# Performance work log

Measured on AMD Instinct MI355X. Metric: run time of the kernel, lower is better.

Reference implementation:

```python
import jax, jax.numpy as jnp
import numpy as np

B, T, D, H = 4, 2048, 1024, 16
HD = D // H
K = 4            # templates per token
VOCAB = 32000


def setup_inputs() -> dict:
    key = jax.random.key(0)
    ks = jax.random.split(key, 6)
    x = jax.random.normal(ks[0], (B, T, D), dtype=jnp.float32)
    sequences = jax.random.randint(ks[1], (B, T, K), 0, VOCAB, dtype=jnp.int64)
    # xavier-uniform-ish scaled weights (torch Linear stores [out, in])
    Wqkv = jax.random.normal(ks[2], (3 * D, D), dtype=jnp.float32) * (1.0 / np.sqrt(D))
    Wout = jax.random.normal(ks[3], (D, D), dtype=jnp.float32) * (1.0 / np.sqrt(D))
    bout = jnp.zeros((D,), dtype=jnp.float32)
    emb = jax.random.normal(ks[4], (VOCAB, D), dtype=jnp.float32) * 0.02
    bias_scale = jnp.asarray(0.1, dtype=jnp.float32)
    return {"x": x, "sequences": sequences, "Wqkv": Wqkv, "Wout": Wout,
            "bout": bout, "emb": emb, "bias_scale": bias_scale}


def reference(x, sequences, Wqkv, Wout, bout, emb, bias_scale):
    b, t, d = x.shape
    h, hd = H, d // H
    # qkv projection (no bias): [B,T,3,H,hd]
    qkv = (x @ Wqkv.T).reshape(b, t, 3, h, hd)
    q = jnp.moveaxis(qkv[:, :, 0], 2, 1)  # [B,H,T,hd]
    k = jnp.moveaxis(qkv[:, :, 1], 2, 1)
    v = jnp.moveaxis(qkv[:, :, 2], 2, 1)
    scale = hd ** -0.5
    scores = jnp.einsum('bhqd,bhkd->bhqk', q, k) * scale  # [B,H,T,T]
    causal = jnp.tril(jnp.ones((t, t), dtype=bool))
    scores = jnp.where(causal[None, None], scores, -jnp.inf)
    w = jax.nn.softmax(scores, axis=-1)
    # dropout p=0.0 -> identity (eval-mode faithful)
    out = jnp.einsum('bhqk,bhkd->bhqd', w, v)
    out = jnp.moveaxis(out, 1, 2).reshape(b, t, d)
    # bias injection: sum template embeddings over template axis
    out = out + emb[sequences].sum(axis=-2) * bias_scale
    return out @ Wout.T + bout
```

## Files before the change

kernel.cpp:

```cpp
#include <hip/hip_runtime.h>
#include <stdint.h>


typedef __attribute__((ext_vector_type(8))) short s16x8;
typedef __attribute__((ext_vector_type(4))) short s16x4;
typedef __attribute__((ext_vector_type(4))) float f32x4;

static __device__ __forceinline__ unsigned short f32_bf16(float f) {
  union { float f; unsigned u; } v; v.f = f;
  unsigned r = v.u + 0x7fffu + ((v.u >> 16) & 1u);
  return (unsigned short)(r >> 16);
}
static __device__ __forceinline__ float bf16_f32(unsigned short h) {
  union { float f; unsigned u; } v; v.u = ((unsigned)h) << 16;
  return v.f;
}
static __device__ __forceinline__ float fexp2(float x) {
#if __has_builtin(__builtin_amdgcn_exp2f)
  return __builtin_amdgcn_exp2f(x);
#else
  return exp2f(x);
#endif
}

__global__ __launch_bounds__(256) void cvt_f32_bf16_k(
    const float* __restrict__ in, unsigned short* __restrict__ out, int n8) {
  int i = blockIdx.x * 256 + threadIdx.x;
  if (i >= n8) return;
  const float4* p = (const float4*)(in + (long)i * 8);
  float4 a = p[0], b = p[1];
  s16x8 o;
  o[0] = (short)f32_bf16(a.x); o[1] = (short)f32_bf16(a.y);
  o[2] = (short)f32_bf16(a.z); o[3] = (short)f32_bf16(a.w);
  o[4] = (short)f32_bf16(b.x); o[5] = (short)f32_bf16(b.y);
  o[6] = (short)f32_bf16(b.z); o[7] = (short)f32_bf16(b.w);
  *(s16x8*)(out + (long)i * 8) = o;
}

__device__ __forceinline__ void glds16(const void* g, void* l) {
  __builtin_amdgcn_global_load_lds(
      (const __attribute__((address_space(1))) void*)g,
      (__attribute__((address_space(3))) void*)l, 16, 0, 0);
}

template <int OUTMODE>
__global__ __launch_bounds__(256) void gemm_bt(
    const unsigned short* __restrict__ A,
    const unsigned short* __restrict__ Bm,
    void* __restrict__ C0, void* __restrict__ C1, void* __restrict__ C2,
    const float* __restrict__ bias, int M, int N, int K) {
  __shared__ unsigned short Asl[128 * 32];
  __shared__ unsigned short Bsl[128 * 32];
  const int tid = threadIdx.x;
  const int l = tid & 63;
  const int w = tid >> 6;
  const int wr = w >> 1, wc = w & 1;
  const int bm = blockIdx.y, bn = blockIdx.x;

  f32x4 acc[4][4] = {};

  const unsigned short* Ag = A + (long)(bm * 128 + w * 16 + (l >> 2)) * K + (l & 3) * 8;
  const unsigned short* Bg = Bm + (long)(bn * 128 + w * 16 + (l >> 2)) * K + (l & 3) * 8;
  unsigned short* Al0 = &Asl[w * 512];
  unsigned short* Bl0 = &Bsl[w * 512];
  const int ro = (l & 15) * 32 + (l >> 4) * 8;

  for (int k0 = 0; k0 < K; k0 += 32) {
    __syncthreads();
    glds16(Ag + k0, Al0);
    glds16(Ag + 64 * K + k0, Al0 + 2048);
    glds16(Bg + k0, Bl0);
    glds16(Bg + 64 * K + k0, Bl0 + 2048);
    __syncthreads();
    s16x8 af[4], bfr[4];
#pragma unroll
    for (int i = 0; i < 4; ++i)
      af[i] = *(const s16x8*)&Asl[(wr * 64 + i * 16) * 32 + ro];
#pragma unroll
    for (int j = 0; j < 4; ++j)
      bfr[j] = *(const s16x8*)&Bsl[(wc * 64 + j * 16) * 32 + ro];
#pragma unroll
    for (int i = 0; i < 4; ++i)
#pragma unroll
      for (int j = 0; j < 4; ++j)
        acc[i][j] = __builtin_amdgcn_mfma_f32_16x16x32_bf16(af[i], bfr[j], acc[i][j], 0, 0, 0);
  }

  const int crow = bm * 128 + wr * 64 + (l >> 4) * 4;
  if (OUTMODE == 2) {
    unsigned short* C = (unsigned short*)(bn < 8 ? C0 : (bn < 16 ? C1 : C2));
    const float qsc = (bn < 8) ? 0.18033688f : 1.0f;
    const int colb = (bn & 7) * 128 + wc * 64 + (l & 15);
#pragma unroll
    for (int i = 0; i < 4; ++i)
#pragma unroll
      for (int j = 0; j < 4; ++j)
#pragma unroll
        for (int r = 0; r < 4; ++r)
          C[(long)(crow + i * 16 + r) * 1024 + colb + j * 16] = f32_bf16(acc[i][j][r] * qsc);
  } else {
    float* C = (float*)C0;
    const int ccol = bn * 128 + wc * 64 + (l & 15);
#pragma unroll
    for (int i = 0; i < 4; ++i)
#pragma unroll
      for (int j = 0; j < 4; ++j) {
        float bv = bias[ccol + j * 16];
#pragma unroll
        for (int r = 0; r < 4; ++r)
          C[(long)(crow + i * 16 + r) * N + ccol + j * 16] = acc[i][j][r] + bv;
      }
  }
}


__device__ __forceinline__ void attn_tile(
    const unsigned short* __restrict__ Ksl, const unsigned short* __restrict__ Vtl,
    unsigned short* Psl, const s16x8* qf, f32x4* o, float* m, float* lpart,
    int qt0, int kv0, bool diag, int w, int g, int d15) {
  f32x4 s[4] = {};
  __builtin_amdgcn_s_setprio(1);
#pragma unroll
  for (int st = 0; st < 4; ++st)
#pragma unroll
    for (int kc = 0; kc < 2; ++kc) {
      s16x8 kf = *(const s16x8*)&Ksl[(st * 16 + d15) * 72 + kc * 32 + g * 8];
      s[st] = __builtin_amdgcn_mfma_f32_16x16x32_bf16(qf[kc], kf, s[st], 0, 0, 0);
    }
  __builtin_amdgcn_s_setprio(0);
#pragma unroll
  for (int r = 0; r < 4; ++r) {
    const int qabs = qt0 + w * 16 + g * 4 + r;
    float sv0 = s[0][r], sv1 = s[1][r], sv2 = s[2][r], sv3 = s[3][r];
    if (diag) {
      if (kv0 + d15 > qabs) sv0 = -1e30f;
      if (kv0 + 16 + d15 > qabs) sv1 = -1e30f;
      if (kv0 + 32 + d15 > qabs) sv2 = -1e30f;
      if (kv0 + 48 + d15 > qabs) sv3 = -1e30f;
    }
    float mx = fmaxf(fmaxf(sv0, sv1), fmaxf(sv2, sv3));
    mx = fmaxf(mx, __shfl_xor(mx, 1));
    mx = fmaxf(mx, __shfl_xor(mx, 2));
    mx = fmaxf(mx, __shfl_xor(mx, 4));
    mx = fmaxf(mx, __shfl_xor(mx, 8));
    const float mn = fmaxf(m[r], mx);
    const float c = fexp2(m[r] - mn);
    m[r] = mn;
    const float p0 = fexp2(sv0 - mn), p1 = fexp2(sv1 - mn);
    const float p2 = fexp2(sv2 - mn), p3 = fexp2(sv3 - mn);
    unsigned short* pr = &Psl[(w * 16 + g * 4 + r) * 72 + d15];
    pr[0] = f32_bf16(p0); pr[16] = f32_bf16(p1);
    pr[32] = f32_bf16(p2); pr[48] = f32_bf16(p3);
    lpart[r] = lpart[r] * c + ((p0 + p1) + (p2 + p3));
#pragma unroll
    for (int ct = 0; ct < 4; ++ct) o[ct][r] *= c;
  }
  __builtin_amdgcn_s_setprio(1);
#pragma unroll
  for (int kc2 = 0; kc2 < 2; ++kc2) {
    s16x8 pf = *(const s16x8*)&Psl[(w * 16 + d15) * 72 + kc2 * 32 + g * 8];
#pragma unroll
    for (int ct = 0; ct < 4; ++ct) {
      s16x8 vf = *(const s16x8*)&Vtl[(ct * 16 + d15) * 72 + ((kc2 * 32 + g * 8) ^ (ct * 8))];
      o[ct] = __builtin_amdgcn_mfma_f32_16x16x32_bf16(pf, vf, o[ct], 0, 0, 0);
    }
  }
  __builtin_amdgcn_s_setprio(0);
}

__global__ __launch_bounds__(256) void attn_k(
    const unsigned short* __restrict__ Qb, const unsigned short* __restrict__ Kb,
    const unsigned short* __restrict__ Vb, unsigned short* __restrict__ attn,
    const int* __restrict__ seq, const float* __restrict__ emb,
    const float* __restrict__ bsc) {
  __shared__ unsigned short Ksl[64 * 72];
  __shared__ unsigned short Vtl[64 * 72];
  __shared__ unsigned short Psl[64 * 72];
  const int tid = threadIdx.x;
  const int l = tid & 63;
  const int w = tid >> 6;
  const int g = l >> 4;
  const int d15 = l & 15;
  const int bx = blockIdx.x;
  const int bh = blockIdx.y;
  const int b = bh >> 4, h = bh & 15;
  const int tok0 = b * 2048;
  const int qA = bx, qB = 31 - bx;
  const int nA = qA + 1, ntiles = qB + 1;
  const unsigned short* Qp = Qb + (long)tok0 * 1024 + h * 64;
  const unsigned short* Kp = Kb + (long)tok0 * 1024 + h * 64;
  const unsigned short* Vp = Vb + (long)tok0 * 1024 + h * 64;

  s16x8 qfA[2], qfB[2];
  {
    const unsigned short* qa = Qp + (long)(qA * 64 + w * 16 + d15) * 1024 + g * 8;
    qfA[0] = *(const s16x8*)qa;
    qfA[1] = *(const s16x8*)(qa + 32);
    const unsigned short* qbp = Qp + (long)(qB * 64 + w * 16 + d15) * 1024 + g * 8;
    qfB[0] = *(const s16x8*)qbp;
    qfB[1] = *(const s16x8*)(qbp + 32);
  }
  f32x4 oA[4] = {}, oB[4] = {};
  float mA[4], lA[4], mB[4], lB[4];
#pragma unroll
  for (int r = 0; r < 4; ++r) {
    mA[r] = -1e30f; lA[r] = 0.f; mB[r] = -1e30f; lB[r] = 0.f;
  }

  const int rs_ = tid >> 2;
  const int c0 = (tid & 3) * 16;
  const int vswz = rs_ ^ ((c0 >> 4) * 8);
  const unsigned short* Kg = Kp + (long)rs_ * 1024 + c0;
  const unsigned short* Vg = Vp + (long)rs_ * 1024 + c0;
  s16x8 kp0 = *(const s16x8*)Kg, kp1 = *(const s16x8*)(Kg + 8);
  s16x8 vp0 = *(const s16x8*)Vg, vp1 = *(const s16x8*)(Vg + 8);

  for (int it = 0; it < ntiles; ++it) {
    __syncthreads();
    *(s16x8*)&Ksl[rs_ * 72 + c0] = kp0;
    *(s16x8*)&Ksl[rs_ * 72 + c0 + 8] = kp1;
#pragma unroll
    for (int e = 0; e < 8; ++e) {
      Vtl[(c0 + e) * 72 + vswz] = (unsigned short)vp0[e];
      Vtl[(c0 + 8 + e) * 72 + vswz] = (unsigned short)vp1[e];
    }
    if (it + 1 < ntiles) {
      Kg += 65536; Vg += 65536;
      kp0 = *(const s16x8*)Kg; kp1 = *(const s16x8*)(Kg + 8);
      vp0 = *(const s16x8*)Vg; vp1 = *(const s16x8*)(Vg + 8);
    }
    __syncthreads();
    attn_tile(Ksl, Vtl, Psl, qfB, oB, mB, lB, qB * 64, it * 64, it == qB, w, g, d15);
    if (it < nA)
      attn_tile(Ksl, Vtl, Psl, qfA, oA, mA, lA, qA * 64, it * 64, it == qA, w, g, d15);
  }

#pragma unroll
  for (int r = 0; r < 4; ++r) {
    float sB = lB[r], sA = lA[r];
    sB += __shfl_xor(sB, 1); sB += __shfl_xor(sB, 2);
    sB += __shfl_xor(sB, 4); sB += __shfl_xor(sB, 8);
    sA += __shfl_xor(sA, 1); sA += __shfl_xor(sA, 2);
    sA += __shfl_xor(sA, 4); sA += __shfl_xor(sA, 8);
    lB[r] = sB; lA[r] = sA;
  }

  const float sc = bsc[0];
  const int colbase = h * 64 + d15;
  const int tB0 = tok0 + qB * 64 + w * 16 + g * 4;
  const int tA0 = tok0 + qA * 64 + w * 16 + g * 4;
  unsigned short* apB = attn + (long)tB0 * 1024 + colbase;
  unsigned short* apA = attn + (long)tA0 * 1024 + colbase;
#pragma unroll
  for (int r = 0; r < 4; ++r) {
    const float invB = 1.0f / lB[r];
    const float invA = 1.0f / lA[r];
    const int* sqB = seq + (long)(tB0 + r) * 4;
    const int* sqA = seq + (long)(tA0 + r) * 4;
    const float* eB0 = emb + (long)sqB[0] * 1024 + colbase;
    const float* eB1 = emb + (long)sqB[1] * 1024 + colbase;
    const float* eB2 = emb + (long)sqB[2] * 1024 + colbase;
    const float* eB3 = emb + (long)sqB[3] * 1024 + colbase;
    const float* eA0 = emb + (long)sqA[0] * 1024 + colbase;
    const float* eA1 = emb + (long)sqA[1] * 1024 + colbase;
    const float* eA2 = emb + (long)sqA[2] * 1024 + colbase;
    const float* eA3 = emb + (long)sqA[3] * 1024 + colbase;
#pragma unroll
    for (int ct = 0; ct < 4; ++ct) {
      const int cc = ct * 16;
      float embB = (eB0[cc] + eB1[cc]) + (eB2[cc] + eB3[cc]);
      float embA = (eA0[cc] + eA1[cc]) + (eA2[cc] + eA3[cc]);
      apB[(long)r * 1024 + cc] = f32_bf16(oB[ct][r] * invB + sc * embB);
      apA[(long)r * 1024 + cc] = f32_bf16(oA[ct][r] * invA + sc * embA);
    }
  }
}

extern "C" void kernel_launch(void* const* d_in, const int* in_sizes, int n_in,
                              void* d_out, int out_size, void* d_ws, size_t ws_size,
                              hipStream_t stream) {
  const float* x = (const float*)d_in[0];
  const int* seq = (const int*)d_in[1];
  const float* Wqkv = (const float*)d_in[2];
  const float* Wout = (const float*)d_in[3];
  const float* bout = (const float*)d_in[4];
  const float* emb = (const float*)d_in[5];
  const float* bsc = (const float*)d_in[6];

  uint8_t* ws = (uint8_t*)d_ws;
  unsigned short* xbf = (unsigned short*)ws;
  unsigned short* wqkvb = (unsigned short*)(ws + 16777216);
  unsigned short* woutb = (unsigned short*)(ws + 23068672);
  unsigned short* Qb = (unsigned short*)(ws + 25165824);
  unsigned short* Kb = (unsigned short*)d_out;
  unsigned short* Vb = Kb + (long)8192 * 1024;

  cvt_f32_bf16_k<<<4096, 256, 0, stream>>>(x, xbf, 1048576);
  cvt_f32_bf16_k<<<1536, 256, 0, stream>>>(Wqkv, wqkvb, 393216);
  cvt_f32_bf16_k<<<512, 256, 0, stream>>>(Wout, woutb, 131072);

  gemm_bt<2><<<dim3(24, 64), 256, 0, stream>>>(xbf, wqkvb, Qb, Kb, Vb, nullptr,
                                               8192, 3072, 1024);
  attn_k<<<dim3(16, 64), 256, 0, stream>>>(Qb, Kb, Vb, xbf, seq, emb, bsc);
  gemm_bt<1><<<dim3(8, 64), 256, 0, stream>>>(xbf, woutb, d_out, nullptr, nullptr,
                                              bout, 8192, 1024, 1024);
}
```

Measured before the change: 435.3 us.

## Process four query tiles per attention block, reusing K/V register fragments

Each attention workgroup now handles two 128-row query stripes (four 64-row sub-tiles) paired from opposite ends of the causal triangle instead of two 64-row tiles. K and V fragments are read from LDS into registers once per KV tile and reused across all active sub-tiles, so LDS reads and global K/V loads per query row go down. The grid is halved, which gives fewer blocks per CU. The larger per-thread state (accumulators, Q and K/V fragments) raises register pressure and may lower occupancy or cause spills.

```diff
diff --git a/kernel.cpp b/kernel.cpp
--- a/kernel.cpp
+++ b/kernel.cpp
@@ -113,60 +113,6 @@
   }
 }
 
-
-__device__ __forceinline__ void attn_tile(
-    const unsigned short* __restrict__ Ksl, const unsigned short* __restrict__ Vtl,
-    unsigned short* Psl, const s16x8* qf, f32x4* o, float* m, float* lpart,
-    int qt0, int kv0, bool diag, int w, int g, int d15) {
-  f32x4 s[4] = {};
-  __builtin_amdgcn_s_setprio(1);
-#pragma unroll
-  for (int st = 0; st < 4; ++st)
-#pragma unroll
-    for (int kc = 0; kc < 2; ++kc) {
-      s16x8 kf = *(const s16x8*)&Ksl[(st * 16 + d15) * 72 + kc * 32 + g * 8];
-      s[st] = __builtin_amdgcn_mfma_f32_16x16x32_bf16(qf[kc], kf, s[st], 0, 0, 0);
-    }
-  __builtin_amdgcn_s_setprio(0);
-#pragma unroll
-  for (int r = 0; r < 4; ++r) {
-    const int qabs = qt0 + w * 16 + g * 4 + r;
-    float sv0 = s[0][r], sv1 = s[1][r], sv2 = s[2][r], sv3 = s[3][r];
-    if (diag) {
-      if (kv0 + d15 > qabs) sv0 = -1e30f;
-      if (kv0 + 16 + d15 > qabs) sv1 = -1e30f;
-      if (kv0 + 32 + d15 > qabs) sv2 = -1e30f;
-      if (kv0 + 48 + d15 > qabs) sv3 = -1e30f;
-    }
-    float mx = fmaxf(fmaxf(sv0, sv1), fmaxf(sv2, sv3));
-    mx = fmaxf(mx, __shfl_xor(mx, 1));
-    mx = fmaxf(mx, __shfl_xor(mx, 2));
-    mx = fmaxf(mx, __shfl_xor(mx, 4));
-    mx = fmaxf(mx, __shfl_xor(mx, 8));
-    const float mn = fmaxf(m[r], mx);
-    const float c = fexp2(m[r] - mn);
-    m[r] = mn;
-    const float p0 = fexp2(sv0 - mn), p1 = fexp2(sv1 - mn);
-    const float p2 = fexp2(sv2 - mn), p3 = fexp2(sv3 - mn);
-    unsigned short* pr = &Psl[(w * 16 + g * 4 + r) * 72 + d15];
-    pr[0] = f32_bf16(p0); pr[16] = f32_bf16(p1);
-    pr[32] = f32_bf16(p2); pr[48] = f32_bf16(p3);
-    lpart[r] = lpart[r] * c + ((p0 + p1) + (p2 + p3));
-#pragma unroll
-    for (int ct = 0; ct < 4; ++ct) o[ct][r] *= c;
-  }
-  __builtin_amdgcn_s_setprio(1);
-#pragma unroll
-  for (int kc2 = 0; kc2 < 2; ++kc2) {
-    s16x8 pf = *(const s16x8*)&Psl[(w * 16 + d15) * 72 + kc2 * 32 + g * 8];
-#pragma unroll
-    for (int ct = 0; ct < 4; ++ct) {
-      s16x8 vf = *(const s16x8*)&Vtl[(ct * 16 + d15) * 72 + ((kc2 * 32 + g * 8) ^ (ct * 8))];
-      o[ct] = __builtin_amdgcn_mfma_f32_16x16x32_bf16(pf, vf, o[ct], 0, 0, 0);
-    }
-  }
-  __builtin_amdgcn_s_setprio(0);
-}
 
 __global__ __launch_bounds__(256) void attn_k(
     const unsigned short* __restrict__ Qb, const unsigned short* __restrict__ Kb,
@@ -185,27 +131,33 @@
   const int bh = blockIdx.y;
   const int b = bh >> 4, h = bh & 15;
   const int tok0 = b * 2048;
-  const int qA = bx, qB = 31 - bx;
-  const int nA = qA + 1, ntiles = qB + 1;
+  const int qt_[2] = {15 - bx, bx};
+  const int ntiles = 2 * qt_[0] + 2;
   const unsigned short* Qp = Qb + (long)tok0 * 1024 + h * 64;
   const unsigned short* Kp = Kb + (long)tok0 * 1024 + h * 64;
   const unsigned short* Vp = Vb + (long)tok0 * 1024 + h * 64;
 
-  s16x8 qfA[2], qfB[2];
-  {
-    const unsigned short* qa = Qp + (long)(qA * 64 + w * 16 + d15) * 1024 + g * 8;
-    qfA[0] = *(const s16x8*)qa;
-    qfA[1] = *(const s16x8*)(qa + 32);
-    const unsigned short* qbp = Qp + (long)(qB * 64 + w * 16 + d15) * 1024 + g * 8;
-    qfB[0] = *(const s16x8*)qbp;
-    qfB[1] = *(const s16x8*)(qbp + 32);
-  }
-  f32x4 oA[4] = {}, oB[4] = {};
-  float mA[4], lA[4], mB[4], lB[4];
-#pragma unroll
-  for (int r = 0; r < 4; ++r) {
-    mA[r] = -1e30f; lA[r] = 0.f; mB[r] = -1e30f; lB[r] = 0.f;
-  }
+  s16x8 qf[2][2][2];
+#pragma unroll
+  for (int t = 0; t < 2; ++t)
+#pragma unroll
+    for (int fi = 0; fi < 2; ++fi) {
+      const unsigned short* qr =
+          Qp + (long)(qt_[t] * 128 + fi * 64 + w * 16 + d15) * 1024 + g * 8;
+      qf[t][fi][0] = *(const s16x8*)qr;
+      qf[t][fi][1] = *(const s16x8*)(qr + 32);
+    }
+  f32x4 o[2][2][4] = {};
+  float m[2][2][4], lp[2][2][4];
+#pragma unroll
+  for (int t = 0; t < 2; ++t)
+#pragma unroll
+    for (int fi = 0; fi < 2; ++fi)
+#pragma unroll
+      for (int r = 0; r < 4; ++r) {
+        m[t][fi][r] = -1e30f;
+        lp[t][fi][r] = 0.f;
+      }
 
   const int rs_ = tid >> 2;
   const int c0 = (tid & 3) * 16;
@@ -216,6 +168,7 @@
   s16x8 vp0 = *(const s16x8*)Vg, vp1 = *(const s16x8*)(Vg + 8);
 
   for (int it = 0; it < ntiles; ++it) {
+    const int kv0 = it * 64;
     __syncthreads();
     *(s16x8*)&Ksl[rs_ * 72 + c0] = kp0;
     *(s16x8*)&Ksl[rs_ * 72 + c0 + 8] = kp1;
@@ -230,50 +183,105 @@
       vp0 = *(const s16x8*)Vg; vp1 = *(const s16x8*)(Vg + 8);
     }
     __syncthreads();
-    attn_tile(Ksl, Vtl, Psl, qfB, oB, mB, lB, qB * 64, it * 64, it == qB, w, g, d15);
-    if (it < nA)
-      attn_tile(Ksl, Vtl, Psl, qfA, oA, mA, lA, qA * 64, it * 64, it == qA, w, g, d15);
-  }
-
-#pragma unroll
-  for (int r = 0; r < 4; ++r) {
-    float sB = lB[r], sA = lA[r];
-    sB += __shfl_xor(sB, 1); sB += __shfl_xor(sB, 2);
-    sB += __shfl_xor(sB, 4); sB += __shfl_xor(sB, 8);
-    sA += __shfl_xor(sA, 1); sA += __shfl_xor(sA, 2);
-    sA += __shfl_xor(sA, 4); sA += __shfl_xor(sA, 8);
-    lB[r] = sB; lA[r] = sA;
+
+    s16x8 kf[8], vf[8];
+#pragma unroll
+    for (int st = 0; st < 4; ++st)
+#pragma unroll
+      for (int kc = 0; kc < 2; ++kc)
+        kf[st * 2 + kc] = *(const s16x8*)&Ksl[(st * 16 + d15) * 72 + kc * 32 + g * 8];
+#pragma unroll
+    for (int kc2 = 0; kc2 < 2; ++kc2)
+#pragma unroll
+      for (int ct = 0; ct < 4; ++ct)
+        vf[kc2 * 4 + ct] =
+            *(const s16x8*)&Vtl[(ct * 16 + d15) * 72 + ((kc2 * 32 + g * 8) ^ (ct * 8))];
+
+#pragma unroll
+    for (int t = 0; t < 2; ++t) {
+      const int qt = qt_[t];
+#pragma unroll
+      for (int fi = 0; fi < 2; ++fi) {
+        const int lim = 2 * qt + fi;
+        if (it > lim) continue;
+        const bool diag = (it == lim);
+        f32x4 s[4] = {};
+        __builtin_amdgcn_s_setprio(1);
+#pragma unroll
+        for (int st = 0; st < 4; ++st)
+#pragma unroll
+          for (int kc = 0; kc < 2; ++kc)
+            s[st] = __builtin_amdgcn_mfma_f32_16x16x32_bf16(
+                qf[t][fi][kc], kf[st * 2 + kc], s[st], 0, 0, 0);
+        __builtin_amdgcn_s_setprio(0);
+#pragma unroll
+        for (int r = 0; r < 4; ++r) {
+          const int qabs = qt * 128 + fi * 64 + w * 16 + g * 4 + r;
+          float sv0 = s[0][r], sv1 = s[1][r], sv2 = s[2][r], sv3 = s[3][r];
+          if (diag) {
+            if (kv0 + d15 > qabs) sv0 = -1e30f;
+            if (kv0 + 16 + d15 > qabs) sv1 = -1e30f;
+            if (kv0 + 32 + d15 > qabs) sv2 = -1e30f;
+            if (kv0 + 48 + d15 > qabs) sv3 = -1e30f;
+          }
+          float mx = fmaxf(fmaxf(sv0, sv1), fmaxf(sv2, sv3));
+          mx = fmaxf(mx, __shfl_xor(mx, 1));
+          mx = fmaxf(mx, __shfl_xor(mx, 2));
+          mx = fmaxf(mx, __shfl_xor(mx, 4));
+          mx = fmaxf(mx, __shfl_xor(mx, 8));
+          const float mn = fmaxf(m[t][fi][r], mx);
+          const float c = fexp2(m[t][fi][r] - mn);
+          m[t][fi][r] = mn;
+          const float p0 = fexp2(sv0 - mn), p1 = fexp2(sv1 - mn);
+          const float p2 = fexp2(sv2 - mn), p3 = fexp2(sv3 - mn);
+          unsigned short* pr = &Psl[(w * 16 + g * 4 + r) * 72 + d15];
+          pr[0] = f32_bf16(p0); pr[16] = f32_bf16(p1);
+          pr[32] = f32_bf16(p2); pr[48] = f32_bf16(p3);
+          lp[t][fi][r] = lp[t][fi][r] * c + ((p0 + p1) + (p2 + p3));
+#pragma unroll
+          for (int ct = 0; ct < 4; ++ct) o[t][fi][ct][r] *= c;
+        }
+        __builtin_amdgcn_s_setprio(1);
+#pragma unroll
+        for (int kc2 = 0; kc2 < 2; ++kc2) {
+          s16x8 pf = *(const s16x8*)&Psl[(w * 16 + d15) * 72 + kc2 * 32 + g * 8];
+#pragma unroll
+          for (int ct = 0; ct < 4; ++ct)
+            o[t][fi][ct] = __builtin_amdgcn_mfma_f32_16x16x32_bf16(
+                pf, vf[kc2 * 4 + ct], o[t][fi][ct], 0, 0, 0);
+        }
+        __builtin_amdgcn_s_setprio(0);
+      }
+    }
   }
 
   const float sc = bsc[0];
   const int colbase = h * 64 + d15;
-  const int tB0 = tok0 + qB * 64 + w * 16 + g * 4;
-  const int tA0 = tok0 + qA * 64 + w * 16 + g * 4;
-  unsigned short* apB = attn + (long)tB0 * 1024 + colbase;
-  unsigned short* apA = attn + (long)tA0 * 1024 + colbase;
-#pragma unroll
-  for (int r = 0; r < 4; ++r) {
-    const float invB = 1.0f / lB[r];
-    const float invA = 1.0f / lA[r];
-    const int* sqB = seq + (long)(tB0 + r) * 4;
-    const int* sqA = seq + (long)(tA0 + r) * 4;
-    const float* eB0 = emb + (long)sqB[0] * 1024 + colbase;
-    const float* eB1 = emb + (long)sqB[1] * 1024 + colbase;
-    const float* eB2 = emb + (long)sqB[2] * 1024 + colbase;
-    const float* eB3 = emb + (long)sqB[3] * 1024 + colbase;
-    const float* eA0 = emb + (long)sqA[0] * 1024 + colbase;
-    const float* eA1 = emb + (long)sqA[1] * 1024 + colbase;
-    const float* eA2 = emb + (long)sqA[2] * 1024 + colbase;
-    const float* eA3 = emb + (long)sqA[3] * 1024 + colbase;
-#pragma unroll
-    for (int ct = 0; ct < 4; ++ct) {
-      const int cc = ct * 16;
-      float embB = (eB0[cc] + eB1[cc]) + (eB2[cc] + eB3[cc]);
-      float embA = (eA0[cc] + eA1[cc]) + (eA2[cc] + eA3[cc]);
-      apB[(long)r * 1024 + cc] = f32_bf16(oB[ct][r] * invB + sc * embB);
-      apA[(long)r * 1024 + cc] = f32_bf16(oA[ct][r] * invA + sc * embA);
-    }
-  }
+#pragma unroll
+  for (int t = 0; t < 2; ++t)
+#pragma unroll
+    for (int fi = 0; fi < 2; ++fi) {
+      const int tk0 = tok0 + qt_[t] * 128 + fi * 64 + w * 16 + g * 4;
+      unsigned short* ap = attn + (long)tk0 * 1024 + colbase;
+#pragma unroll
+      for (int r = 0; r < 4; ++r) {
+        float ls = lp[t][fi][r];
+        ls += __shfl_xor(ls, 1); ls += __shfl_xor(ls, 2);
+        ls += __shfl_xor(ls, 4); ls += __shfl_xor(ls, 8);
+        const float inv = 1.0f / ls;
+        const int* sq = seq + (long)(tk0 + r) * 4;
+        const float* e0 = emb + (long)sq[0] * 1024 + colbase;
+        const float* e1 = emb + (long)sq[1] * 1024 + colbase;
+        const float* e2 = emb + (long)sq[2] * 1024 + colbase;
+        const float* e3 = emb + (long)sq[3] * 1024 + colbase;
+#pragma unroll
+        for (int ct = 0; ct < 4; ++ct) {
+          const int cc = ct * 16;
+          float ev = (e0[cc] + e1[cc]) + (e2[cc] + e3[cc]);
+          ap[(long)r * 1024 + cc] = f32_bf16(o[t][fi][ct][r] * inv + sc * ev);
+        }
+      }
+    }
 }
 
 extern "C" void kernel_launch(void* const* d_in, const int* in_sizes, int n_in,
@@ -301,7 +309,7 @@
 
   gemm_bt<2><<<dim3(24, 64), 256, 0, stream>>>(xbf, wqkvb, Qb, Kb, Vb, nullptr,
                                                8192, 3072, 1024);
-  attn_k<<<dim3(16, 64), 256, 0, stream>>>(Qb, Kb, Vb, xbf, seq, emb, bsc);
+  attn_k<<<dim3(8, 64), 256, 0, stream>>>(Qb, Kb, Vb, xbf, seq, emb, bsc);
   gemm_bt<1><<<dim3(8, 64), 256, 0, stream>>>(xbf, woutb, d_out, nullptr, nullptr,
                                               bout, 8192, 1024, 1024);
 }
```

After: 518.6 us. +19.1%, slower.
